# Kernel optimization log

Hardware: AMD Instinct MI355X
Metric: run time of the kernel (lower is better)

Reference implementation:

```python
import jax, jax.numpy as jnp
import numpy as np

POOL = 7          # pool_size (hardcoded 7x7 bins in source)
TOTAL_BINS = POOL * POOL  # 49
ALPHA = 32        # channels per position-sensitive group
NUM_ROIS = 8192
H = W = 20        # feature-map size; source hardcodes img_w=img_h=20 for normalization
CROP = 2          # bin_crop_size = 14 // 7


def setup_inputs() -> dict:
    key = jax.random.key(0)
    k1, k2, k3 = jax.random.split(key, 3)
    img = jax.random.normal(k1, (1, H, W, TOTAL_BINS * ALPHA), dtype=jnp.float32)
    xy = jax.random.uniform(k2, (1, NUM_ROIS, 2), minval=0.0, maxval=14.0, dtype=jnp.float32)
    wh = jax.random.uniform(k3, (1, NUM_ROIS, 2), minval=2.0, maxval=6.0, dtype=jnp.float32)
    rois = jnp.concatenate([xy, wh], axis=-1)  # (1, R, 4) as (x, y, w, h)
    return {"img": img, "rois": rois}


def _ps_roi_align(img, rois):
    R = rois.shape[1]
    x, y, w, h = rois[0, :, 0], rois[0, :, 1], rois[0, :, 2], rois[0, :, 3]
    step_y = h / POOL
    step_x = w / POOL

    # bin index b = bin_x * POOL + bin_y (outer loop bin_x, inner bin_y in source)
    bin_x = jnp.repeat(jnp.arange(POOL, dtype=jnp.float32), POOL)  # (49,)
    bin_y = jnp.tile(jnp.arange(POOL, dtype=jnp.float32), POOL)    # (49,)

    # normalized box coords [y1, x1, y2, x2] per (bin, roi)
    y1 = (y[None, :] + bin_y[:, None] * step_y[None, :]) / 20.0          # (49, R)
    x1 = (x[None, :] + bin_x[:, None] * step_x[None, :]) / 20.0
    y2 = (y[None, :] + (bin_y[:, None] + 1.0) * step_y[None, :]) / 20.0
    x2 = (x[None, :] + (bin_x[:, None] + 1.0) * step_x[None, :]) / 20.0

    # tf.image.crop_and_resize with crop size (2,2): sample points are exactly
    # the box corners in pixel space: y1*(H-1), y2*(H-1) (and same for x).
    ys = jnp.stack([y1, y2], axis=-1) * (H - 1)  # (49, R, 2)
    xs = jnp.stack([x1, x2], axis=-1) * (W - 1)  # (49, R, 2)

    valid_y = (ys >= 0) & (ys <= H - 1)  # (49, R, 2)
    valid_x = (xs >= 0) & (xs <= W - 1)

    fy = jnp.floor(ys)
    fx = jnp.floor(xs)
    wy = ys - fy  # bilinear lerp weights
    wx = xs - fx
    y0i = jnp.clip(fy.astype(jnp.int32), 0, H - 1)
    y1i = jnp.clip(y0i + 1, 0, H - 1)
    x0i = jnp.clip(fx.astype(jnp.int32), 0, W - 1)
    x1i = jnp.clip(x0i + 1, 0, W - 1)

    # split channels into 49 position-sensitive groups of ALPHA: (49, H, W, ALPHA)
    f = img[0].reshape(H, W, TOTAL_BINS, ALPHA).transpose(2, 0, 1, 3)

    bidx = jnp.arange(TOTAL_BINS)[:, None, None, None]  # (49,1,1,1)
    Y0 = y0i[:, :, :, None]  # (49, R, 2, 1)
    Y1 = y1i[:, :, :, None]
    X0 = x0i[:, :, None, :]  # (49, R, 1, 2)
    X1 = x1i[:, :, None, :]

    v00 = f[bidx, Y0, X0]  # (49, R, 2, 2, ALPHA)
    v01 = f[bidx, Y0, X1]
    v10 = f[bidx, Y1, X0]
    v11 = f[bidx, Y1, X1]

    WY = wy[:, :, :, None, None]  # (49, R, 2, 1, 1)
    WX = wx[:, :, None, :, None]  # (49, R, 1, 2, 1)
    val = (v00 * (1 - WY) * (1 - WX) + v01 * (1 - WY) * WX
           + v10 * WY * (1 - WX) + v11 * WY * WX)

    mask = (valid_y[:, :, :, None] & valid_x[:, :, None, :])[..., None]
    val = jnp.where(mask, val, 0.0)

    pooled = val.mean(axis=(2, 3))  # (49, R, ALPHA), mean over 2x2 crop
    # concat along bin axis then reshape: out[0, r, bin_x, bin_y, a]
    out = pooled.transpose(1, 0, 2).reshape(1, R, POOL, POOL, ALPHA)
    return out


def reference(img, rois):
    return _ps_roi_align(img, rois)
```

## Files before the change

### kernel.cpp

```cpp
#include <hip/hip_runtime.h>


#define NBIN 49
#define CH 1568
#define IMG_W 20

typedef float vf4 __attribute__((ext_vector_type(4)));

__device__ __forceinline__ void axis_weights(float s0, float s1,
                                             int& b, float& W0, float& W1, float& W2)
{
    const float f0 = floorf(s0), f1 = floorf(s1);
    const float w0 = s0 - f0,    w1 = s1 - f1;
    const float v0 = (s0 >= 0.f && s0 <= 19.f) ? 1.f : 0.f;
    const float v1 = (s1 >= 0.f && s1 <= 19.f) ? 1.f : 0.f;
    const int c00 = min(max((int)f0, 0), 19);
    const int c01 = min(c00 + 1, 19);
    const int c10 = min(max((int)f1, 0), 19);
    const int c11 = min(c10 + 1, 19);
    b = c00;
    W0 = v0 * (1.f - w0);
    W1 = 0.f; W2 = 0.f;
    float t = v0 * w0;
    if (c01 == b) W0 += t; else W1 += t;
    t = v1 * (1.f - w1);
    if (c10 == b) W0 += t; else W1 += t;
    t = v1 * w1;
    const int d = c11 - b;
    W0 += (d == 0) ? t : 0.f;
    W1 += (d == 1) ? t : 0.f;
    W2 += (d == 2) ? t : 0.f;
}

__global__ __launch_bounds__(256) void psroi_kernel(
    const float* __restrict__ img,
    const float* __restrict__ rois,
    float* __restrict__ out)
{
    const unsigned tid = blockIdx.x * 256u + threadIdx.x;
    const unsigned g   = tid >> 3;
    const unsigned a4  = (tid & 7u) << 2;
    const unsigned r   = g / 49u;
    const unsigned bin = g - r * 49u;
    const unsigned p   = bin / 7u;
    const unsigned q   = bin - p * 7u;

    const vf4 roi = ((const vf4*)rois)[r];
    const float x = roi.x, y = roi.y, w = roi.z, h = roi.w;
    const float step_x = w * (1.0f / 7.0f);
    const float step_y = h * (1.0f / 7.0f);
    const float s = 19.0f / 20.0f;

    const float sx0 = (x + (float)p * step_x) * s;
    const float sx1 = (x + (float)(p + 1) * step_x) * s;
    const float sy0 = (y + (float)q * step_y) * s;
    const float sy1 = (y + (float)(q + 1) * step_y) * s;

    int bx, by;
    float WX0, WX1, WX2, WY0, WY1, WY2;
    axis_weights(sx0, sx1, bx, WX0, WX1, WX2);
    axis_weights(sy0, sy1, by, WY0, WY1, WY2);
    WY0 *= 0.25f; WY1 *= 0.25f; WY2 *= 0.25f;

    const float WX[3] = { WX0, WX1, WX2 };
    const float WY[3] = { WY0, WY1, WY2 };
    const int col[3] = { bx, min(bx + 1, 19), min(bx + 2, 19) };
    const int row[3] = { by, min(by + 1, 19), min(by + 2, 19) };

    const float* base = img + bin * 32u + a4;
    vf4 acc = { 0.f, 0.f, 0.f, 0.f };

#pragma unroll
    for (int i = 0; i < 3; ++i) {
        const float* rp = base + (size_t)row[i] * (IMG_W * CH);
#pragma unroll
        for (int j = 0; j < 3; ++j) {
            const vf4 v = *(const vf4*)(rp + (size_t)col[j] * CH);
            const float wgt = WY[i] * WX[j];
            acc += wgt * v;
        }
    }

    __builtin_nontemporal_store(acc, (vf4*)(out + (size_t)g * 32u + a4));
}

extern "C" void kernel_launch(void* const* d_in, const int* in_sizes, int n_in,
                              void* d_out, int out_size, void* d_ws, size_t ws_size,
                              hipStream_t stream) {
    const float* img  = (const float*)d_in[0];
    const float* rois = (const float*)d_in[1];
    float* out = (float*)d_out;
    hipLaunchKernelGGL(psroi_kernel, dim3(12544), dim3(256), 0, stream, img, rois, out);
}
```

Before: 85.50 us.

## Stage per-bin image slice and ROI weights in LDS, one bin per block

New measurement: 86.14 us. No clear change (+0.7%).

```diff
diff --git a/kernel.cpp b/kernel.cpp
--- a/kernel.cpp
+++ b/kernel.cpp
@@ -1,9 +1,12 @@
 #include <hip/hip_runtime.h>
 
 
-#define NBIN 49
 #define CH 1568
 #define IMG_W 20
+#define CELLS 400
+#define IMG_F (CELLS * 32)
+#define PKOFF IMG_F
+#define ROIS_PER_BLOCK 256
 
 typedef float vf4 __attribute__((ext_vector_type(4)));
 
@@ -37,51 +40,81 @@
     const float* __restrict__ rois,
     float* __restrict__ out)
 {
-    const unsigned tid = blockIdx.x * 256u + threadIdx.x;
-    const unsigned g   = tid >> 3;
-    const unsigned a4  = (tid & 7u) << 2;
-    const unsigned r   = g / 49u;
-    const unsigned bin = g - r * 49u;
-    const unsigned p   = bin / 7u;
-    const unsigned q   = bin - p * 7u;
+    __shared__ float lds[IMG_F + ROIS_PER_BLOCK * 8];
 
-    const vf4 roi = ((const vf4*)rois)[r];
-    const float x = roi.x, y = roi.y, w = roi.z, h = roi.w;
-    const float step_x = w * (1.0f / 7.0f);
-    const float step_y = h * (1.0f / 7.0f);
-    const float s = 19.0f / 20.0f;
+    const unsigned t     = threadIdx.x;
+    const unsigned bin   = blockIdx.x % 49u;
+    const unsigned chunk = blockIdx.x / 49u;
+    const unsigned p     = bin / 7u;
+    const unsigned q     = bin - p * 7u;
 
-    const float sx0 = (x + (float)p * step_x) * s;
-    const float sx1 = (x + (float)(p + 1) * step_x) * s;
-    const float sy0 = (y + (float)q * step_y) * s;
-    const float sy1 = (y + (float)(q + 1) * step_y) * s;
-
-    int bx, by;
-    float WX0, WX1, WX2, WY0, WY1, WY2;
-    axis_weights(sx0, sx1, bx, WX0, WX1, WX2);
-    axis_weights(sy0, sy1, by, WY0, WY1, WY2);
-    WY0 *= 0.25f; WY1 *= 0.25f; WY2 *= 0.25f;
-
-    const float WX[3] = { WX0, WX1, WX2 };
-    const float WY[3] = { WY0, WY1, WY2 };
-    const int col[3] = { bx, min(bx + 1, 19), min(bx + 2, 19) };
-    const int row[3] = { by, min(by + 1, 19), min(by + 2, 19) };
-
-    const float* base = img + bin * 32u + a4;
-    vf4 acc = { 0.f, 0.f, 0.f, 0.f };
-
-#pragma unroll
-    for (int i = 0; i < 3; ++i) {
-        const float* rp = base + (size_t)row[i] * (IMG_W * CH);
-#pragma unroll
-        for (int j = 0; j < 3; ++j) {
-            const vf4 v = *(const vf4*)(rp + (size_t)col[j] * CH);
-            const float wgt = WY[i] * WX[j];
-            acc += wgt * v;
+    {
+        const float* src = img + bin * 32u;
+        for (unsigned idx = t; idx < CELLS * 8u; idx += 256u) {
+            const unsigned cell = idx >> 3;
+            const unsigned sub  = idx & 7u;
+            const vf4 v = *(const vf4*)(src + (size_t)cell * CH + sub * 4u);
+            *(vf4*)(&lds[cell * 32u + sub * 4u]) = v;
         }
     }
 
-    __builtin_nontemporal_store(acc, (vf4*)(out + (size_t)g * 32u + a4));
+    {
+        const unsigned r = chunk * ROIS_PER_BLOCK + t;
+        const vf4 roi = ((const vf4*)rois)[r];
+        const float step_x = roi.z * (1.0f / 7.0f);
+        const float step_y = roi.w * (1.0f / 7.0f);
+        const float s = 19.0f / 20.0f;
+        const float sx0 = (roi.x + (float)p * step_x) * s;
+        const float sx1 = (roi.x + (float)(p + 1) * step_x) * s;
+        const float sy0 = (roi.y + (float)q * step_y) * s;
+        const float sy1 = (roi.y + (float)(q + 1) * step_y) * s;
+
+        int bx, by;
+        float WX0, WX1, WX2, WY0, WY1, WY2;
+        axis_weights(sx0, sx1, bx, WX0, WX1, WX2);
+        axis_weights(sy0, sy1, by, WY0, WY1, WY2);
+
+        vf4 p0, p1;
+        p0.x = __int_as_float(bx);
+        p0.y = __int_as_float(by);
+        p0.z = WX0; p0.w = WX1;
+        p1.x = WX2;
+        p1.y = WY0 * 0.25f; p1.z = WY1 * 0.25f; p1.w = WY2 * 0.25f;
+        *(vf4*)(&lds[PKOFF + t * 8u])     = p0;
+        *(vf4*)(&lds[PKOFF + t * 8u + 4]) = p1;
+    }
+
+    __syncthreads();
+
+    const unsigned gl = t >> 3;
+    const unsigned a4 = (t & 7u) << 2;
+    const size_t out_base = ((size_t)chunk * ROIS_PER_BLOCK) * (49u * 32u) + bin * 32u + a4;
+
+#pragma unroll
+    for (unsigned k = 0; k < 8; ++k) {
+        const unsigned rl = k * 32u + gl;
+        const float* pkp = &lds[PKOFF + rl * 8u];
+        const vf4 p0 = *(const vf4*)pkp;
+        const vf4 p1 = *(const vf4*)(pkp + 4);
+        const int bx = __float_as_int(p0.x);
+        const int by = __float_as_int(p0.y);
+        const float WX[3] = { p0.z, p0.w, p1.x };
+        const float WY[3] = { p1.y, p1.z, p1.w };
+        const int col[3] = { bx, min(bx + 1, 19), min(bx + 2, 19) };
+        const int row[3] = { by, min(by + 1, 19), min(by + 2, 19) };
+
+        vf4 acc = { 0.f, 0.f, 0.f, 0.f };
+#pragma unroll
+        for (int i = 0; i < 3; ++i) {
+            const unsigned rowbase = (unsigned)row[i] * IMG_W;
+#pragma unroll
+            for (int j = 0; j < 3; ++j) {
+                const vf4 v = *(const vf4*)(&lds[(rowbase + (unsigned)col[j]) * 32u + a4]);
+                acc += (WY[i] * WX[j]) * v;
+            }
+        }
+        __builtin_nontemporal_store(acc, (vf4*)(out + out_base + (size_t)rl * (49u * 32u)));
+    }
 }
 
 extern "C" void kernel_launch(void* const* d_in, const int* in_sizes, int n_in,
@@ -90,5 +123,5 @@
     const float* img  = (const float*)d_in[0];
     const float* rois = (const float*)d_in[1];
     float* out = (float*)d_out;
-    hipLaunchKernelGGL(psroi_kernel, dim3(12544), dim3(256), 0, stream, img, rois, out);
+    hipLaunchKernelGGL(psroi_kernel, dim3(1568), dim3(256), 0, stream, img, rois, out);
 }
```
